# Performance work log

Measured on AMD Instinct MI355X. Metric: run time of the kernel, lower is better.

The kernel has to match this reference:

```python
import jax, jax.numpy as jnp
import numpy as np

B, S, D = 2, 2048, 4096
N_HEADS, N_KV_HEADS, HEAD_DIM = 32, 8, 128
Q_DIM = N_HEADS * HEAD_DIM        # 4096
KV_DIM = N_KV_HEADS * HEAD_DIM    # 1024
N_REP = N_HEADS // N_KV_HEADS
ROPE_THETA = 500000.0


def make_freqs_cis(seqlen, head_dim, theta):
    # Interleaved (sin, cos) pairs per rotary frequency, matching the module's
    # einsum/flip RoPE convention: row1 = x0*sin + x1*cos, row0 = x0*cos - x1*sin.
    inv_freq = 1.0 / (theta ** (np.arange(0, head_dim, 2, dtype=np.float32) / head_dim))
    t = np.arange(seqlen, dtype=np.float32)
    ang = np.outer(t, inv_freq)                       # [S, hd/2]
    fc = np.stack([np.sin(ang), np.cos(ang)], axis=-1)  # [S, hd/2, 2]
    return jnp.asarray(fc.reshape(seqlen, head_dim))


def apply_rotary_emb(xq, xk, freqs_cis):
    # xq: [B,S,Hq,hd], xk: [B,S,Hkv,hd], freqs_cis: [S,hd]
    xq_shape, xk_shape = xq.shape, xk.shape
    xq2 = xq.reshape(*xq.shape[:-1], -1, 2)
    xk2 = xk.reshape(*xk.shape[:-1], -1, 2)
    fc = freqs_cis.reshape(freqs_cis.shape[0], 1, -1, 2)   # [S,1,hd/2,2]
    # row_1 = <x, fc>
    xq_row1 = jnp.einsum('bshpi,shpi->bshp', xq2, fc)
    xk_row1 = jnp.einsum('bshpi,shpi->bshp', xk2, fc)
    # flipped fc with negated second component: (f1, -f0)
    fc_flip = jnp.flip(fc, axis=-1) * jnp.array([1.0, -1.0], dtype=fc.dtype)
    xq_row0 = jnp.einsum('bshpi,shpi->bshp', xq2, fc_flip)
    xk_row0 = jnp.einsum('bshpi,shpi->bshp', xk2, fc_flip)
    xq_out = jnp.stack([xq_row0, xq_row1], axis=-1).reshape(xq_shape)
    xk_out = jnp.stack([xk_row0, xk_row1], axis=-1).reshape(xk_shape)
    return xq_out, xk_out


def setup_inputs() -> dict:
    key = jax.random.key(0)
    k1, k2, k3 = jax.random.split(key, 3)
    x = jax.random.normal(k1, (B, S, D), dtype=jnp.float32)
    wqkv = jax.random.normal(k2, (D, Q_DIM + 2 * KV_DIM), dtype=jnp.float32) * 0.02
    wo = jax.random.normal(k3, (Q_DIM, D), dtype=jnp.float32) * 0.02
    freqs_cis = make_freqs_cis(S, HEAD_DIM, ROPE_THETA)
    return {"x": x, "freqs_cis": freqs_cis, "wqkv": wqkv, "wo": wo, "is_causal": 1}


def reference(x, freqs_cis, wqkv, wo, is_causal):
    bsz, seqlen, _ = x.shape
    xqkv = jnp.einsum('bsd,de->bse', x, wqkv)
    xq = xqkv[..., :Q_DIM].reshape(bsz, seqlen, N_HEADS, HEAD_DIM)
    xk = xqkv[..., Q_DIM:Q_DIM + KV_DIM].reshape(bsz, seqlen, N_KV_HEADS, HEAD_DIM)
    xv = xqkv[..., Q_DIM + KV_DIM:].reshape(bsz, seqlen, N_KV_HEADS, HEAD_DIM)
    xq, xk = apply_rotary_emb(xq, xk, freqs_cis)
    # [B,H,S,hd]
    xq = xq.transpose(0, 2, 1, 3)
    xk = jnp.repeat(xk.transpose(0, 2, 1, 3), N_REP, axis=1)
    xv = jnp.repeat(xv.transpose(0, 2, 1, 3), N_REP, axis=1)
    scale = 1.0 / jnp.sqrt(jnp.asarray(HEAD_DIM, dtype=xq.dtype))
    scores = jnp.einsum('bhqd,bhkd->bhqk', xq, xk) * scale
    if is_causal:
        mask = jnp.tril(jnp.ones((seqlen, seqlen), dtype=bool))
        scores = jnp.where(mask, scores, jnp.finfo(scores.dtype).min)
    attn = jax.nn.softmax(scores, axis=-1)
    out = jnp.einsum('bhqk,bhkd->bhqd', attn, xv)
    out = out.transpose(0, 2, 1, 3).reshape(bsz, seqlen, Q_DIM)
    return jnp.einsum('bsd,de->bse', out, wo)
```

## Files before the change

kernel.cpp:

```cpp
#include <hip/hip_runtime.h>
#include <stdint.h>
#include <stddef.h>

#define BB 2
#define SS 2048
#define DD 4096
#define NH 32
#define NKV 8
#define HD 128
#define QDIM 4096
#define KVDIM 1024
#define NQKV 6144
#define NTILES 64
#define QK_SCALE_L2E 0.12751744f

typedef __bf16 bf16;
typedef __bf16 bf16x8 __attribute__((ext_vector_type(8)));
typedef __bf16 bf16x4 __attribute__((ext_vector_type(4)));
typedef float f32x4 __attribute__((ext_vector_type(4)));

#define MFMA16(a, b, c) __builtin_amdgcn_mfma_f32_16x16x32_bf16((a), (b), (c), 0, 0, 0)
#define VMW5() asm volatile("s_waitcnt vmcnt(5)" ::: "memory")
#define VMW4() asm volatile("s_waitcnt vmcnt(4)" ::: "memory")
#define VMW2() asm volatile("s_waitcnt vmcnt(2)" ::: "memory")
#define VMW0() asm volatile("s_waitcnt vmcnt(0)" ::: "memory")
#define BARX()                                  \
    do {                                        \
        __builtin_amdgcn_s_barrier();           \
        __builtin_amdgcn_sched_barrier(0);      \
    } while (0)
#define LGKM0_SGB()                                         \
    do {                                                    \
        asm volatile("s_waitcnt lgkmcnt(0)" ::: "memory");  \
        __builtin_amdgcn_sched_barrier(0);                  \
    } while (0)

typedef __attribute__((address_space(1))) void GASV;
typedef __attribute__((address_space(3))) void LASV;

__device__ __forceinline__ void gload_lds16(const void* g, void* l) {
    __builtin_amdgcn_global_load_lds((GASV*)g, (LASV*)l, 16, 0, 0);
}

__device__ __forceinline__ float fexp2(float x) {
    float r;
    asm("v_exp_f32 %0, %1" : "=v"(r) : "v"(x));
    return r;
}

__global__ __launch_bounds__(256) void k_cvt_x(const float* __restrict__ in,
                                               bf16* __restrict__ out) {
    size_t i = ((size_t)blockIdx.x * 256 + threadIdx.x) * 8;
    const float4 a = *(const float4*)(in + i);
    const float4 b = *(const float4*)(in + i + 4);
    bf16x8 v;
    v[0] = (bf16)a.x; v[1] = (bf16)a.y; v[2] = (bf16)a.z; v[3] = (bf16)a.w;
    v[4] = (bf16)b.x; v[5] = (bf16)b.y; v[6] = (bf16)b.z; v[7] = (bf16)b.w;
    *(bf16x8*)(out + i) = v;
}

__global__ __launch_bounds__(256) void k_tr_cvt(const float* __restrict__ in,
                                                bf16* __restrict__ out, int R, int C) {
    __shared__ float tile[128][65];
    const int t = threadIdx.x;
    const int tx = t & 15, ty = t >> 4;
    const int r0 = blockIdx.y * 128, c0 = blockIdx.x * 64;
#pragma unroll
    for (int p = 0; p < 8; ++p) {
        const float4 v = *(const float4*)(in + (size_t)(r0 + p * 16 + ty) * C + c0 + tx * 4);
        tile[p * 16 + ty][tx * 4 + 0] = v.x;
        tile[p * 16 + ty][tx * 4 + 1] = v.y;
        tile[p * 16 + ty][tx * 4 + 2] = v.z;
        tile[p * 16 + ty][tx * 4 + 3] = v.w;
    }
    __syncthreads();
#pragma unroll
    for (int q = 0; q < 4; ++q) {
        const int lc = q * 16 + ty;
        bf16x8 pk;
#pragma unroll
        for (int jx = 0; jx < 8; ++jx) pk[jx] = (bf16)tile[tx * 8 + jx][lc];
        *(bf16x8*)(out + (size_t)(c0 + lc) * R + r0 + tx * 8) = pk;
    }
}

__device__ __forceinline__ void stage_half(char* ldsRegion, const bf16* gsrc) {
    const int t = threadIdx.x;
    const int wid = t >> 6;
#pragma unroll
    for (int i = 0; i < 2; ++i) {
        const int off = i * 8192 + t * 16;
        const int row = off >> 7;
        const int pc = (off >> 4) & 7;
        const int lc = pc ^ (row & 7);
        gload_lds16(gsrc + (size_t)row * 4096 + lc * 8,
                    ldsRegion + i * 8192 + wid * 1024);
    }
}

__device__ __forceinline__ void gemm256(const bf16* __restrict__ At,
                                        const bf16* __restrict__ Bt,
                                        char* LB, f32x4 acc[8][4]) {
    const int tid = threadIdx.x, lane = tid & 63, wid = tid >> 6;
    const int wm = wid >> 2, wn = wid & 3;
    const int l15 = lane & 15, l4 = lane >> 4;

    const f32x4 vz = {0.f, 0.f, 0.f, 0.f};
#pragma unroll
    for (int m = 0; m < 8; ++m)
#pragma unroll
        for (int n = 0; n < 4; ++n) acc[m][n] = vz;

    auto Areg = [&](int db, int h) -> char* { return LB + db * 32768 + h * 16384; };
    auto Breg = [&](int db, int h) -> char* { return LB + 65536 + db * 32768 + h * 16384; };

    bf16x8 RA[2][4], RAb[2][4], RB0[2][2], RB1[2][2];

    auto loadA = [&](bf16x8 dst[2][4], int db, int h) {
        char* base = Areg(db, h);
#pragma unroll
        for (int kk = 0; kk < 2; ++kk)
#pragma unroll
            for (int mf = 0; mf < 4; ++mf) {
                const int row = wm * 64 + mf * 16 + l15;
                const int cc = kk * 4 + l4;
                dst[kk][mf] = *(const bf16x8*)(base + row * 128 + ((cc ^ (row & 7)) << 4));
            }
    };
    auto loadB = [&](bf16x8 dst[2][2], int db, int h) {
        char* base = Breg(db, h);
#pragma unroll
        for (int kk = 0; kk < 2; ++kk)
#pragma unroll
            for (int nf = 0; nf < 2; ++nf) {
                const int row = wn * 32 + nf * 16 + l15;
                const int cc = kk * 4 + l4;
                dst[kk][nf] = *(const bf16x8*)(base + row * 128 + ((cc ^ (row & 7)) << 4));
            }
    };
    auto stA = [&](int tau, int h) {
        stage_half(Areg(tau & 1, h), At + (size_t)(h * 128) * 4096 + tau * 64);
    };
    auto stB = [&](int tau, int h) {
        stage_half(Breg(tau & 1, h), Bt + (size_t)(h * 128) * 4096 + tau * 64);
    };
    auto mma = [&](bf16x8 A[2][4], bf16x8 B[2][2], int mb, int nb) {
        __builtin_amdgcn_s_setprio(1);
#pragma unroll
        for (int kk = 0; kk < 2; ++kk)
#pragma unroll
            for (int mf = 0; mf < 4; ++mf)
#pragma unroll
                for (int nf = 0; nf < 2; ++nf)
                    acc[mb + mf][nb + nf] = MFMA16(A[kk][mf], B[kk][nf], acc[mb + mf][nb + nf]);
        __builtin_amdgcn_s_setprio(0);
    };

    stA(0, 0); stB(0, 0);
    stB(0, 1); stA(0, 1);
    VMW4();
    BARX();

#pragma unroll 1
    for (int tau = 0; tau < NTILES - 1; ++tau) {
        const int db = tau & 1;
        loadA(RA, db, 0);
        loadB(RB0, db, 0);
        stA(tau + 1, 0);
        stB(tau + 1, 0);
        VMW4();
        BARX(); LGKM0_SGB();
        mma(RA, RB0, 0, 0);
        BARX();
        loadB(RB1, db, 1);
        stB(tau + 1, 1);
        stA(tau + 1, 1);
        BARX(); LGKM0_SGB();
        mma(RA, RB1, 0, 2);
        BARX();
        loadA(RAb, db, 1);
        VMW4();
        BARX(); LGKM0_SGB();
        mma(RAb, RB0, 4, 0);
        mma(RAb, RB1, 4, 2);
        BARX();
    }

    VMW0();
    BARX();
    {
        const int db = (NTILES - 1) & 1;
        loadA(RA, db, 0);
        loadB(RB0, db, 0);
        mma(RA, RB0, 0, 0);
        loadB(RB1, db, 1);
        mma(RA, RB1, 0, 2);
        loadA(RAb, db, 1);
        mma(RAb, RB0, 4, 0);
        mma(RAb, RB1, 4, 2);
    }
}

__device__ __forceinline__ void stage_B192(char* ldsRegion, const bf16* gsrc) {
    const int t = threadIdx.x;
    const int wid = t >> 6;
#pragma unroll
    for (int i = 0; i < 3; ++i) {
        const int off = i * 8192 + t * 16;
        const int row = off >> 7;
        const int pc = (off >> 4) & 7;
        const int lc = pc ^ (row & 7);
        gload_lds16(gsrc + (size_t)row * 4096 + lc * 8,
                    ldsRegion + i * 8192 + wid * 1024);
    }
}

__device__ __forceinline__ void gemm192(const bf16* __restrict__ At,
                                        const bf16* __restrict__ Bt,
                                        char* LB, f32x4 acc[8][3]) {
    const int tid = threadIdx.x, lane = tid & 63, wid = tid >> 6;
    const int wm = wid >> 2, wn = wid & 3;
    const int l15 = lane & 15, l4 = lane >> 4;

    const f32x4 vz = {0.f, 0.f, 0.f, 0.f};
#pragma unroll
    for (int m = 0; m < 8; ++m)
#pragma unroll
        for (int n = 0; n < 3; ++n) acc[m][n] = vz;

    auto Areg = [&](int db, int h) -> char* { return LB + db * 32768 + h * 16384; };
    auto Breg = [&](int db) -> char* { return LB + 65536 + db * 24576; };

    bf16x8 RA[2][4], RAb[2][4], RB0[2][2], RB1[2];

    auto loadA = [&](bf16x8 dst[2][4], int db, int h) {
        char* base = Areg(db, h);
#pragma unroll
        for (int kk = 0; kk < 2; ++kk)
#pragma unroll
            for (int mf = 0; mf < 4; ++mf) {
                const int row = wm * 64 + mf * 16 + l15;
                const int cc = kk * 4 + l4;
                dst[kk][mf] = *(const bf16x8*)(base + row * 128 + ((cc ^ (row & 7)) << 4));
            }
    };
    auto loadB0 = [&](int db) {
        char* base = Breg(db);
#pragma unroll
        for (int kk = 0; kk < 2; ++kk)
#pragma unroll
            for (int nf = 0; nf < 2; ++nf) {
                const int row = wn * 48 + nf * 16 + l15;
                const int cc = kk * 4 + l4;
                RB0[kk][nf] = *(const bf16x8*)(base + row * 128 + ((cc ^ (row & 7)) << 4));
            }
    };
    auto loadB1 = [&](int db) {
        char* base = Breg(db);
#pragma unroll
        for (int kk = 0; kk < 2; ++kk) {
            const int row = wn * 48 + 32 + l15;
            const int cc = kk * 4 + l4;
            RB1[kk] = *(const bf16x8*)(base + row * 128 + ((cc ^ (row & 7)) << 4));
        }
    };
    auto stA = [&](int tau, int h) {
        stage_half(Areg(tau & 1, h), At + (size_t)(h * 128) * 4096 + tau * 64);
    };
    auto stB = [&](int tau) {
        stage_B192(Breg(tau & 1), Bt + tau * 64);
    };
    auto mmaB0 = [&](bf16x8 A[2][4], int mb) {
        __builtin_amdgcn_s_setprio(1);
#pragma unroll
        for (int kk = 0; kk < 2; ++kk)
#pragma unroll
            for (int mf = 0; mf < 4; ++mf)
#pragma unroll
                for (int nf = 0; nf < 2; ++nf)
                    acc[mb + mf][nf] = MFMA16(A[kk][mf], RB0[kk][nf], acc[mb + mf][nf]);
        __builtin_amdgcn_s_setprio(0);
    };
    auto mmaB1 = [&](bf16x8 A[2][4], int mb) {
        __builtin_amdgcn_s_setprio(1);
#pragma unroll
        for (int kk = 0; kk < 2; ++kk)
#pragma unroll
            for (int mf = 0; mf < 4; ++mf)
                acc[mb + mf][2] = MFMA16(A[kk][mf], RB1[kk], acc[mb + mf][2]);
        __builtin_amdgcn_s_setprio(0);
    };

    stA(0, 0); stB(0);
    stA(0, 1);
    VMW2();
    BARX();

#pragma unroll 1
    for (int tau = 0; tau < NTILES - 1; ++tau) {
        const int db = tau & 1;
        loadA(RA, db, 0);
        loadB0(db);
        stA(tau + 1, 0);
        stB(tau + 1);
        VMW5();
        BARX(); LGKM0_SGB();
        mmaB0(RA, 0);
        BARX();
        loadB1(db);
        stA(tau + 1, 1);
        BARX(); LGKM0_SGB();
        mmaB1(RA, 0);
        BARX();
        loadA(RAb, db, 1);
        VMW2();
        BARX(); LGKM0_SGB();
        mmaB0(RAb, 4);
        mmaB1(RAb, 4);
        BARX();
    }

    VMW0();
    BARX();
    {
        const int db = (NTILES - 1) & 1;
        loadA(RA, db, 0);
        loadB0(db);
        mmaB0(RA, 0);
        loadB1(db);
        mmaB1(RA, 0);
        loadA(RAb, db, 1);
        mmaB0(RAb, 4);
        mmaB1(RAb, 4);
    }
}

__device__ __forceinline__ void xcd_swizzle(int gx, int& bx, int& by) {
    const int nwg = gx * gridDim.y;
    int lin = by * gx + bx;
    lin = (lin & 7) * (nwg >> 3) + (lin >> 3);
    bx = lin % gx;
    by = lin / gx;
}

__global__ __launch_bounds__(512, 2) void k_gemm_qkv(const bf16* __restrict__ A,
                                                     const bf16* __restrict__ Bt,
                                                     const float* __restrict__ fc,
                                                     bf16* __restrict__ Qb,
                                                     bf16* __restrict__ Kb,
                                                     bf16* __restrict__ VTb) {
    __shared__ __align__(16) char LB[114688];
    f32x4 acc[8][3];
    int bx = blockIdx.x, by = blockIdx.y;
    xcd_swizzle(NQKV / 192, bx, by);
    gemm192(A + (size_t)by * 256 * 4096, Bt + (size_t)bx * 192 * 4096, LB, acc);

    const int tid = threadIdx.x, lane = tid & 63, wid = tid >> 6;
    const int wm = wid >> 2, wn = wid & 3;
    const int l15 = lane & 15, l4 = lane >> 4;
#pragma unroll
    for (int mf = 0; mf < 8; ++mf) {
        const int rowbase = by * 256 + (mf >> 2) * 128 + wm * 64 + (mf & 3) * 16 + l4 * 4;
#pragma unroll
        for (int nf = 0; nf < 3; ++nf) {
            const int rb = bx * 192 + wn * 48 + nf * 16;
            const int col = rb + l15;
            f32x4 v = acc[mf][nf];
            if (rb < QDIM + KVDIM) {
                const int d = col & (HD - 1);
                const int dp = d & ~1;
                const float sgn = (d & 1) ? 1.f : -1.f;
#pragma unroll
                for (int r = 0; r < 4; ++r) {
                    const int row = rowbase + r;
                    const int s = row & (SS - 1);
                    const float2 sc = *(const float2*)(fc + s * HD + dp);
                    const float partner = __shfl_xor(v[r], 1);
                    float res = v[r] * sc.y + sgn * partner * sc.x;
                    if (rb < QDIM) {
                        res *= QK_SCALE_L2E;
                        Qb[(size_t)row * QDIM + col] = (bf16)res;
                    } else {
                        Kb[(size_t)row * KVDIM + (col - QDIM)] = (bf16)res;
                    }
                }
            } else {
                const int hdv = col - (QDIM + KVDIM);
                const int kvh = hdv >> 7, dd = hdv & (HD - 1);
                const int bb = rowbase >> 11, s = rowbase & (SS - 1);
                bf16x4 pk;
#pragma unroll
                for (int r = 0; r < 4; ++r) pk[r] = (bf16)v[r];
                *(bf16x4*)(VTb + ((size_t)((bb * NKV + kvh) * HD + dd)) * SS + s) = pk;
            }
        }
    }
}

__global__ __launch_bounds__(512, 2) void k_gemm_out(const bf16* __restrict__ A,
                                                     const bf16* __restrict__ Bt,
                                                     float* __restrict__ out) {
    __shared__ __align__(16) char LB[131072];
    f32x4 acc[8][4];
    int bx = blockIdx.x, by = blockIdx.y;
    xcd_swizzle(DD / 256, bx, by);
    gemm256(A + (size_t)by * 256 * 4096, Bt + (size_t)bx * 256 * 4096, LB, acc);

    const int tid = threadIdx.x, lane = tid & 63, wid = tid >> 6;
    const int wm = wid >> 2, wn = wid & 3;
    const int l15 = lane & 15, l4 = lane >> 4;
#pragma unroll
    for (int mf = 0; mf < 8; ++mf) {
        const int row = by * 256 + (mf >> 2) * 128 + wm * 64 + (mf & 3) * 16 + l4 * 4;
#pragma unroll
        for (int nf = 0; nf < 4; ++nf) {
            const int col = bx * 256 + (nf >> 1) * 128 + wn * 32 + (nf & 1) * 16 + l15;
#pragma unroll
            for (int r = 0; r < 4; ++r) out[(size_t)(row + r) * DD + col] = acc[mf][nf][r];
        }
    }
}

__global__ __launch_bounds__(256, 2) void k_attn(const bf16* __restrict__ Qb,
                                                 const bf16* __restrict__ Kb,
                                                 const bf16* __restrict__ VTb,
                                                 bf16* __restrict__ Ob) {
    __shared__ __align__(16) bf16 Ks[64 * 128];
    __shared__ __align__(16) bf16 Vs[128 * 64];
    __shared__ __align__(16) bf16 Ps[4][32 * 88];
    int lin = (blockIdx.z * NH + blockIdx.y) * 8 + blockIdx.x;
    lin = (lin & 7) * 64 + (lin >> 3);
    const int jj = lin & 7, h = (lin >> 3) & (NH - 1), b = lin >> 8;
    const int kvh = h >> 2;
    const int tid = threadIdx.x, lane = tid & 63, w = tid >> 6;
    const int l15 = lane & 15, l4 = lane >> 4;

    const bf16* Kg = Kb + (size_t)b * SS * KVDIM + kvh * HD;
    const bf16* Vg = VTb + (size_t)(b * NKV + kvh) * HD * SS;

    int4 kreg[4], vreg[4];
    const f32x4 vz = {0.f, 0.f, 0.f, 0.f};

    auto issue_kv = [&](int t) {
#pragma unroll
        for (int i = 0; i < 4; ++i) {
            const int off = i * 4096 + tid * 16;
            const int row = off >> 8;
            const int cc = (off >> 4) & 15;
            kreg[i] = *(const int4*)((const char*)(Kg + (size_t)(t * 64 + row) * KVDIM) + cc * 16);
        }
#pragma unroll
        for (int i = 0; i < 4; ++i) {
            const int off = i * 4096 + tid * 16;
            const int row = off >> 7;
            const int cc = (off >> 4) & 7;
            vreg[i] = *(const int4*)((const char*)(Vg + (size_t)row * SS + t * 64) + cc * 16);
        }
    };

#pragma unroll 1
    for (int pj = 0; pj < 2; ++pj) {
        const int j = pj ? (15 - jj) : jj;
        const int q0 = j * 128;
        const int nt = 2 * j + 2;

        bf16x8 qf[2][4];
#pragma unroll
        for (int m = 0; m < 2; ++m) {
            const int qrow = q0 + w * 32 + m * 16 + l15;
            const bf16* qb = Qb + ((size_t)(b * SS + qrow) << 12) + h * HD + l4 * 8;
#pragma unroll
            for (int kc = 0; kc < 4; ++kc) qf[m][kc] = *(const bf16x8*)(qb + kc * 32);
        }

        f32x4 o[2][8];
#pragma unroll
        for (int m = 0; m < 2; ++m)
#pragma unroll
            for (int df = 0; df < 8; ++df) o[m][df] = vz;
        float m_run[2][4], l_run[2][4];
#pragma unroll
        for (int m = 0; m < 2; ++m)
#pragma unroll
            for (int r = 0; r < 4; ++r) { m_run[m][r] = -1e30f; l_run[m][r] = 0.f; }

        issue_kv(0);

        for (int t = 0; t < nt; ++t) {
            __syncthreads();
#pragma unroll
            for (int i = 0; i < 4; ++i) {
                const int off = i * 4096 + tid * 16;
                const int row = off >> 8;
                const int cc = (off >> 4) & 15;
                const int lc = cc ^ (row & 7);
                *(int4*)((char*)Ks + row * 256 + lc * 16) = kreg[i];
            }
#pragma unroll
            for (int i = 0; i < 4; ++i) {
                const int off = i * 4096 + tid * 16;
                const int row = off >> 7;
                const int cc = (off >> 4) & 7;
                const int lc = cc ^ (row & 7);
                *(int4*)((char*)Vs + row * 128 + lc * 16) = vreg[i];
            }
            __syncthreads();

            if (t + 1 < nt) issue_kv(t + 1);

            f32x4 sa[2][4];
#pragma unroll
            for (int m = 0; m < 2; ++m)
#pragma unroll
                for (int n = 0; n < 4; ++n) sa[m][n] = vz;
            __builtin_amdgcn_s_setprio(1);
#pragma unroll
            for (int kc = 0; kc < 4; ++kc)
#pragma unroll
                for (int n = 0; n < 4; ++n) {
                    const int krow = n * 16 + l15;
                    const int cc = kc * 4 + l4;
                    const bf16x8 kf =
                        *(const bf16x8*)((const char*)Ks + (krow << 8) + ((cc ^ (krow & 7)) << 4));
                    sa[0][n] = MFMA16(qf[0][kc], kf, sa[0][n]);
                    sa[1][n] = MFMA16(qf[1][kc], kf, sa[1][n]);
                }
            __builtin_amdgcn_s_setprio(0);

            if (t >= 2 * j) {
#pragma unroll
                for (int m = 0; m < 2; ++m)
#pragma unroll
                    for (int n = 0; n < 4; ++n)
#pragma unroll
                        for (int r = 0; r < 4; ++r) {
                            const int col = t * 64 + n * 16 + l15;
                            const int qr = q0 + w * 32 + m * 16 + l4 * 4 + r;
                            if (col > qr) sa[m][n][r] = -1e30f;
                        }
            }

#pragma unroll
            for (int m = 0; m < 2; ++m)
#pragma unroll
                for (int r = 0; r < 4; ++r) {
                    float mx = fmaxf(fmaxf(sa[m][0][r], sa[m][1][r]),
                                     fmaxf(sa[m][2][r], sa[m][3][r]));
#pragma unroll
                    for (int mk = 1; mk <= 8; mk <<= 1) mx = fmaxf(mx, __shfl_xor(mx, mk));
                    const float mn = fmaxf(m_run[m][r], mx);
                    const float alpha = fexp2(m_run[m][r] - mn);
                    m_run[m][r] = mn;
                    float rs = 0.f;
#pragma unroll
                    for (int n = 0; n < 4; ++n) {
                        const float p = fexp2(sa[m][n][r] - mn);
                        sa[m][n][r] = p;
                        rs += p;
                    }
#pragma unroll
                    for (int mk = 1; mk <= 8; mk <<= 1) rs += __shfl_xor(rs, mk);
                    l_run[m][r] = l_run[m][r] * alpha + rs;
#pragma unroll
                    for (int df = 0; df < 8; ++df) o[m][df][r] *= alpha;
                }

#pragma unroll
            for (int m = 0; m < 2; ++m)
#pragma unroll
                for (int n = 0; n < 4; ++n)
#pragma unroll
                    for (int r = 0; r < 4; ++r)
                        Ps[w][(m * 16 + l4 * 4 + r) * 88 + n * 16 + l15] = (bf16)sa[m][n][r];

            bf16x8 pf0[2], pf1[2];
#pragma unroll
            for (int ks = 0; ks < 2; ++ks) {
                pf0[ks] = *(const bf16x8*)(&Ps[w][l15 * 88 + ks * 32 + l4 * 8]);
                pf1[ks] = *(const bf16x8*)(&Ps[w][(16 + l15) * 88 + ks * 32 + l4 * 8]);
            }

            __builtin_amdgcn_s_setprio(1);
#pragma unroll
            for (int df = 0; df < 8; ++df)
#pragma unroll
                for (int ks = 0; ks < 2; ++ks) {
                    const int vrow = df * 16 + l15;
                    const int cc = ks * 4 + l4;
                    const bf16x8 vf =
                        *(const bf16x8*)((const char*)Vs + (vrow << 7) + ((cc ^ (vrow & 7)) << 4));
                    o[0][df] = MFMA16(pf0[ks], vf, o[0][df]);
                    o[1][df] = MFMA16(pf1[ks], vf, o[1][df]);
                }
            __builtin_amdgcn_s_setprio(0);
        }

#pragma unroll
        for (int m = 0; m < 2; ++m)
#pragma unroll
            for (int r = 0; r < 4; ++r) {
                const float inv = 1.f / l_run[m][r];
                const size_t row = (size_t)(b * SS + q0 + w * 32 + m * 16 + l4 * 4 + r);
#pragma unroll
                for (int df = 0; df < 8; ++df)
                    Ob[(row << 12) + h * HD + df * 16 + l15] = (bf16)(o[m][df][r] * inv);
            }
    }
}

extern "C" void kernel_launch(void* const* d_in, const int* in_sizes, int n_in,
                              void* d_out, int out_size, void* d_ws, size_t ws_size,
                              hipStream_t stream) {
    const float* x    = (const float*)d_in[0];
    const float* fc   = (const float*)d_in[1];
    const float* wqkv = (const float*)d_in[2];
    const float* wo   = (const float*)d_in[3];

    char* wsp = (char*)d_ws;
    const size_t MB = (size_t)1 << 20;
    bf16* xb    = (bf16*)(wsp);
    bf16* wqkvT = (bf16*)(wsp + 32 * MB);
    bf16* woT   = (bf16*)(wsp + 32 * MB);
    bf16* Qb    = (bf16*)(wsp + 80 * MB);
    bf16* Kb    = (bf16*)(wsp + 112 * MB);
    bf16* VTb   = (bf16*)(wsp + 120 * MB);
    bf16* Ab    = (bf16*)(wsp);
    float* out  = (float*)d_out;

    k_cvt_x<<<8192, 256, 0, stream>>>(x, xb);
    k_tr_cvt<<<dim3(NQKV / 64, DD / 128), 256, 0, stream>>>(wqkv, wqkvT, DD, NQKV);
    k_gemm_qkv<<<dim3(NQKV / 192, (BB * SS) / 256), 512, 0, stream>>>(xb, wqkvT, fc, Qb, Kb, VTb);
    k_tr_cvt<<<dim3(DD / 64, QDIM / 128), 256, 0, stream>>>(wo, woT, QDIM, DD);
    k_attn<<<dim3(8, NH, BB), 256, 0, stream>>>(Qb, Kb, VTb, Ab);
    k_gemm_out<<<dim3(DD / 256, (BB * SS) / 256), 512, 0, stream>>>(Ab, woT, out);
}
```

Measured before the change: 570.3 us.

## Defer softmax max rescaling in attention and swizzle GEMM grids column-major

```diff
diff --git a/kernel.cpp b/kernel.cpp
--- a/kernel.cpp
+++ b/kernel.cpp
@@ -13,6 +13,7 @@
 #define NQKV 6144
 #define NTILES 64
 #define QK_SCALE_L2E 0.12751744f
+#define DEFER_THR 11.5f
 
 typedef __bf16 bf16;
 typedef __bf16 bf16x8 __attribute__((ext_vector_type(8)));
@@ -335,12 +336,13 @@
     }
 }
 
-__device__ __forceinline__ void xcd_swizzle(int gx, int& bx, int& by) {
-    const int nwg = gx * gridDim.y;
-    int lin = by * gx + bx;
+__device__ __forceinline__ void xcd_swizzle(int& bx, int& by) {
+    const int gx = gridDim.x, gy = gridDim.y;
+    const int nwg = gx * gy;
+    int lin = bx * gy + by;
     lin = (lin & 7) * (nwg >> 3) + (lin >> 3);
-    bx = lin % gx;
-    by = lin / gx;
+    bx = lin / gy;
+    by = lin % gy;
 }
 
 __global__ __launch_bounds__(512, 2) void k_gemm_qkv(const bf16* __restrict__ A,
@@ -352,7 +354,7 @@
     __shared__ __align__(16) char LB[114688];
     f32x4 acc[8][3];
     int bx = blockIdx.x, by = blockIdx.y;
-    xcd_swizzle(NQKV / 192, bx, by);
+    xcd_swizzle(bx, by);
     gemm192(A + (size_t)by * 256 * 4096, Bt + (size_t)bx * 192 * 4096, LB, acc);
 
     const int tid = threadIdx.x, lane = tid & 63, wid = tid >> 6;
@@ -403,7 +405,7 @@
     __shared__ __align__(16) char LB[131072];
     f32x4 acc[8][4];
     int bx = blockIdx.x, by = blockIdx.y;
-    xcd_swizzle(DD / 256, bx, by);
+    xcd_swizzle(bx, by);
     gemm256(A + (size_t)by * 256 * 4096, Bt + (size_t)bx * 256 * 4096, LB, acc);
 
     const int tid = threadIdx.x, lane = tid & 63, wid = tid >> 6;
@@ -540,6 +542,8 @@
                         }
             }
 
+            float mxv[2][4];
+            bool need = false;
 #pragma unroll
             for (int m = 0; m < 2; ++m)
 #pragma unroll
@@ -548,22 +552,47 @@
                                      fmaxf(sa[m][2][r], sa[m][3][r]));
 #pragma unroll
                     for (int mk = 1; mk <= 8; mk <<= 1) mx = fmaxf(mx, __shfl_xor(mx, mk));
-                    const float mn = fmaxf(m_run[m][r], mx);
-                    const float alpha = fexp2(m_run[m][r] - mn);
-                    m_run[m][r] = mn;
-                    float rs = 0.f;
-#pragma unroll
-                    for (int n = 0; n < 4; ++n) {
-                        const float p = fexp2(sa[m][n][r] - mn);
-                        sa[m][n][r] = p;
-                        rs += p;
+                    mxv[m][r] = mx;
+                    need = need || (mx > m_run[m][r] + DEFER_THR);
+                }
+            if (__any(need)) {
+#pragma unroll
+                for (int m = 0; m < 2; ++m)
+#pragma unroll
+                    for (int r = 0; r < 4; ++r) {
+                        const float mn = fmaxf(m_run[m][r], mxv[m][r]);
+                        const float alpha = fexp2(m_run[m][r] - mn);
+                        m_run[m][r] = mn;
+                        float rs = 0.f;
+#pragma unroll
+                        for (int n = 0; n < 4; ++n) {
+                            const float p = fexp2(sa[m][n][r] - mn);
+                            sa[m][n][r] = p;
+                            rs += p;
+                        }
+#pragma unroll
+                        for (int mk = 1; mk <= 8; mk <<= 1) rs += __shfl_xor(rs, mk);
+                        l_run[m][r] = l_run[m][r] * alpha + rs;
+#pragma unroll
+                        for (int df = 0; df < 8; ++df) o[m][df][r] *= alpha;
                     }
-#pragma unroll
-                    for (int mk = 1; mk <= 8; mk <<= 1) rs += __shfl_xor(rs, mk);
-                    l_run[m][r] = l_run[m][r] * alpha + rs;
-#pragma unroll
-                    for (int df = 0; df < 8; ++df) o[m][df][r] *= alpha;
-                }
+            } else {
+#pragma unroll
+                for (int m = 0; m < 2; ++m)
+#pragma unroll
+                    for (int r = 0; r < 4; ++r) {
+                        float rs = 0.f;
+#pragma unroll
+                        for (int n = 0; n < 4; ++n) {
+                            const float p = fexp2(sa[m][n][r] - m_run[m][r]);
+                            sa[m][n][r] = p;
+                            rs += p;
+                        }
+#pragma unroll
+                        for (int mk = 1; mk <= 8; mk <<= 1) rs += __shfl_xor(rs, mk);
+                        l_run[m][r] += rs;
+                    }
+            }
 
 #pragma unroll
             for (int m = 0; m < 2; ++m)
```

Result: slower. 871.3 us (+52.8%).
